# Kernel optimization log

Hardware: AMD Instinct MI355X
Metric: run time of the kernel (lower is better)

## Reference

```python
import jax, jax.numpy as jnp
import numpy as np

HIDDEN = 896
N_HEADS = 14
N_KV = 2
HEAD_DIM = HIDDEN // N_HEADS  # 64
N_REP = N_HEADS // N_KV       # 7
ROPE_THETA = 1000000.0


def setup_inputs() -> dict:
    key = jax.random.key(0)
    ks = jax.random.split(key, 8)
    B, S = 2, 2048
    s = 0.02
    return {
        "hidden_states": jax.random.normal(ks[0], (B, S, HIDDEN), dtype=jnp.float32),
        "position_ids": jnp.broadcast_to(jnp.arange(S, dtype=jnp.int64), (B, S)),
        "Wq": jax.random.normal(ks[1], (HIDDEN, HIDDEN), dtype=jnp.float32) * s,
        "bq": jnp.zeros((HIDDEN,), dtype=jnp.float32),
        "Wk": jax.random.normal(ks[2], (N_KV * HEAD_DIM, HIDDEN), dtype=jnp.float32) * s,
        "bk": jnp.zeros((N_KV * HEAD_DIM,), dtype=jnp.float32),
        "Wv": jax.random.normal(ks[3], (N_KV * HEAD_DIM, HIDDEN), dtype=jnp.float32) * s,
        "bv": jnp.zeros((N_KV * HEAD_DIM,), dtype=jnp.float32),
        "Wo": jax.random.normal(ks[4], (HIDDEN, HIDDEN), dtype=jnp.float32) * s,
    }


def _rotate_half(x):
    x1, x2 = x[..., : HEAD_DIM // 2], x[..., HEAD_DIM // 2 :]
    return jnp.concatenate((-x2, x1), axis=-1)


def reference(hidden_states, position_ids, Wq, bq, Wk, bk, Wv, bv, Wo):
    B, S, _ = hidden_states.shape
    q = (hidden_states @ Wq.T + bq).reshape(B, S, N_HEADS, HEAD_DIM)
    k = (hidden_states @ Wk.T + bk).reshape(B, S, N_KV, HEAD_DIM)
    v = (hidden_states @ Wv.T + bv).reshape(B, S, N_KV, HEAD_DIM)

    # RoPE: cos/sin [B, S, 1, HEAD_DIM]
    inv_freq = 1.0 / (ROPE_THETA ** (jnp.arange(0, HEAD_DIM, 2, dtype=jnp.float32) / HEAD_DIM))
    freqs = position_ids.astype(jnp.float32)[..., None] * inv_freq  # [B,S,D/2]
    emb = jnp.concatenate((freqs, freqs), axis=-1)
    cos = jnp.cos(emb)[:, :, None, :]
    sin = jnp.sin(emb)[:, :, None, :]
    q = q * cos + _rotate_half(q) * sin
    k = k * cos + _rotate_half(k) * sin

    # [B, H, S, D]; repeat KV heads (GQA)
    q = q.transpose(0, 2, 1, 3)
    k = jnp.repeat(k.transpose(0, 2, 1, 3), N_REP, axis=1)
    v = jnp.repeat(v.transpose(0, 2, 1, 3), N_REP, axis=1)

    scale = 1.0 / np.sqrt(HEAD_DIM)
    scores = jnp.einsum("bhqd,bhkd->bhqk", q, k) * scale
    causal = jnp.tril(jnp.ones((S, S), dtype=bool))
    scores = jnp.where(causal[None, None, :, :], scores, jnp.finfo(scores.dtype).min)
    probs = jax.nn.softmax(scores, axis=-1)
    attn = jnp.einsum("bhqk,bhkd->bhqd", probs, v)  # [B,H,S,D]
    attn = attn.transpose(0, 2, 1, 3).reshape(B, S, HIDDEN)
    return attn @ Wo.T
```

## Files before the change

kernel.cpp:

```cpp
#include <hip/hip_runtime.h>

#define HID 896
#define NH 14
#define NKV 2
#define NREP 7
#define SEQ 2048
#define BT 2
#define NTOK (BT*SEQ)
#define CSCALE 0.18033688011112042f

typedef __attribute__((ext_vector_type(8))) short bf16x8;
typedef __attribute__((ext_vector_type(8))) unsigned short u16x8;
typedef __attribute__((ext_vector_type(4))) float fx4;
typedef __attribute__((ext_vector_type(4))) short s16x4;
typedef _Float16 f16x4 __attribute__((ext_vector_type(4)));
typedef __fp16 fp16x2 __attribute__((ext_vector_type(2)));

__device__ __forceinline__ unsigned short f2b(float x){
  union { float f; unsigned u; } a; a.f = x;
  unsigned r = a.u + 0x7FFFu + ((a.u >> 16) & 1u);
  return (unsigned short)(r >> 16);
}
__device__ __forceinline__ unsigned short f2h(float x){
  union { _Float16 h; unsigned short u; } a; a.h = (_Float16)x; return a.u;
}
__device__ __forceinline__ u16x8 cvt8(float4 a, float4 b){
  u16x8 o;
  o[0]=f2b(a.x); o[1]=f2b(a.y); o[2]=f2b(a.z); o[3]=f2b(a.w);
  o[4]=f2b(b.x); o[5]=f2b(b.y); o[6]=f2b(b.z); o[7]=f2b(b.w);
  return o;
}

__global__ __launch_bounds__(256) void qkv_gemm_kernel(
    const float* __restrict__ hidden,
    const float* __restrict__ Wq, const float* __restrict__ Wk, const float* __restrict__ Wv,
    const float* __restrict__ bq, const float* __restrict__ bk, const float* __restrict__ bv,
    const int* __restrict__ pos,
    unsigned short* __restrict__ qo, unsigned short* __restrict__ ko,
    unsigned short* __restrict__ vt)
{
  __shared__ short As[64*72];
  __shared__ short Bs[128*72];
  const int tid = threadIdx.x;
  const int bm = blockIdx.x, bn = blockIdx.y;
  const int w = tid >> 6, l = tid & 63, l15 = l & 15, q4 = l >> 4;
  const int wm = w >> 1, wn = w & 1;

  fx4 acc[2][4] = {};

  const float* Wsrc = (bn < 7) ? Wq + (size_t)(bn*128)*HID : ((bn == 7) ? Wk : Wv);

  const int srow = tid >> 3, scol = (tid & 7)*8;
  const float* Agf = hidden + (size_t)(bm*64 + srow)*HID + scol;
  const float* Bgf = Wsrc + (size_t)srow*HID + scol;

  float4 a0[2], a1[2], b0[4], b1[4];
#pragma unroll
  for (int p = 0; p < 2; p++){
    a0[p] = *(const float4*)(Agf + (size_t)p*32*HID);
    a1[p] = *(const float4*)(Agf + (size_t)p*32*HID + 4);
  }
#pragma unroll
  for (int p = 0; p < 4; p++){
    b0[p] = *(const float4*)(Bgf + (size_t)p*32*HID);
    b1[p] = *(const float4*)(Bgf + (size_t)p*32*HID + 4);
  }

  for (int kt = 0; kt < 14; kt++){
#pragma unroll
    for (int p = 0; p < 2; p++)
      *(u16x8*)&As[(srow + p*32)*72 + scol] = cvt8(a0[p], a1[p]);
#pragma unroll
    for (int p = 0; p < 4; p++)
      *(u16x8*)&Bs[(srow + p*32)*72 + scol] = cvt8(b0[p], b1[p]);
    __syncthreads();
    if (kt < 13){
      const int ko_ = (kt+1)*64;
#pragma unroll
      for (int p = 0; p < 2; p++){
        a0[p] = *(const float4*)(Agf + (size_t)p*32*HID + ko_);
        a1[p] = *(const float4*)(Agf + (size_t)p*32*HID + ko_ + 4);
      }
#pragma unroll
      for (int p = 0; p < 4; p++){
        b0[p] = *(const float4*)(Bgf + (size_t)p*32*HID + ko_);
        b1[p] = *(const float4*)(Bgf + (size_t)p*32*HID + ko_ + 4);
      }
    }
#pragma unroll
    for (int ks = 0; ks < 2; ks++){
      bf16x8 af[2], bf[4];
#pragma unroll
      for (int mt = 0; mt < 2; mt++)
        af[mt] = *(bf16x8*)&As[(wm*32 + mt*16 + l15)*72 + ks*32 + q4*8];
#pragma unroll
      for (int nt = 0; nt < 4; nt++)
        bf[nt] = *(bf16x8*)&Bs[(wn*64 + nt*16 + l15)*72 + ks*32 + q4*8];
#pragma unroll
      for (int mt = 0; mt < 2; mt++)
#pragma unroll
        for (int nt = 0; nt < 4; nt++)
          acc[mt][nt] = __builtin_amdgcn_mfma_f32_16x16x32_bf16(af[mt], bf[nt], acc[mt][nt], 0,0,0);
    }
    __syncthreads();
  }

  const int hu = bn*2 + wn;
  const float* bias; int kind, hloc;
  if (hu < NH)      { bias = bq + hu*64;      kind = 0; hloc = hu; }
  else if (hu < 16) { bias = bk + (hu-NH)*64; kind = 1; hloc = hu-NH; }
  else              { bias = bv + (hu-16)*64; kind = 2; hloc = hu-16; }
  float bl[4];
#pragma unroll
  for (int nt = 0; nt < 4; nt++) bl[nt] = bias[nt*16 + l15];

  if (kind == 2){
#pragma unroll
    for (int mt = 0; mt < 2; mt++)
#pragma unroll
      for (int j = 0; j < 4; j++){
        int grow = bm*64 + wm*32 + mt*16 + q4*4 + j;
        int b = grow >> 11, s = grow & (SEQ-1);
        int tile = s >> 6, key = s & 63;
        unsigned short* dst = vt + (size_t)(((b*NKV + hloc)*(SEQ/64) + tile)*4096);
#pragma unroll
        for (int nt = 0; nt < 4; nt++)
          dst[(nt*16 + l15)*64 + key] = f2h(acc[mt][nt][j] + bl[nt]);
      }
  } else {
    const float qs = (kind == 0) ? CSCALE : 1.0f;
    float invf[2];
#pragma unroll
    for (int nt = 0; nt < 2; nt++)
      invf[nt] = exp2f(-(float)(nt*16 + l15) * 0.62286151779138041f);
#pragma unroll
    for (int mt = 0; mt < 2; mt++)
#pragma unroll
      for (int j = 0; j < 4; j++){
        int grow = bm*64 + wm*32 + mt*16 + q4*4 + j;
        int b = grow >> 11, s = grow & (SEQ-1);
        float p = (float)pos[grow];
        unsigned short* dst = (kind == 0)
            ? qo + ((size_t)(b*NH  + hloc)*SEQ + s)*64
            : ko + ((size_t)(b*NKV + hloc)*SEQ + s)*64;
        float x1 = acc[mt][0][j] + bl[0], x2 = acc[mt][2][j] + bl[2];
        float y1 = acc[mt][1][j] + bl[1], y2 = acc[mt][3][j] + bl[3];
        float s0v, c0v, s1v, c1v;
        sincosf(p*invf[0], &s0v, &c0v);
        sincosf(p*invf[1], &s1v, &c1v);
        dst[l15]      = f2b((x1*c0v - x2*s0v)*qs);
        dst[16 + l15] = f2b((y1*c1v - y2*s1v)*qs);
        dst[32 + l15] = f2b((x2*c0v + x1*s0v)*qs);
        dst[48 + l15] = f2b((y2*c1v + y1*s1v)*qs);
      }
  }
}

__device__ __forceinline__ void smax_pv(
    const fx4* s, bool diag, int wl, int q4,
    float& m_run, float& l_run, fx4* o, const f16x4 vf[4][4])
{
  float tv[16];
#pragma unroll
  for (int tl = 0; tl < 4; tl++)
#pragma unroll
    for (int j = 0; j < 4; j++){
      float x = s[tl][j];
      if (diag && (tl*16 + q4*4 + j > wl)) x = -1e30f;
      tv[tl*4+j] = x;
    }
  float mx = tv[0];
#pragma unroll
  for (int i = 1; i < 16; i++) mx = fmaxf(mx, tv[i]);
  mx = fmaxf(mx, __shfl_xor(mx, 16));
  mx = fmaxf(mx, __shfl_xor(mx, 32));
  float mn = fmaxf(m_run, mx);
  float al = exp2f(m_run - mn);
  m_run = mn;
  float p[16], rs = 0.f;
#pragma unroll
  for (int i = 0; i < 16; i++){ p[i] = exp2f(tv[i] - mn); rs += p[i]; }
  rs += __shfl_xor(rs, 16);
  rs += __shfl_xor(rs, 32);
  l_run = l_run*al + rs;
#pragma unroll
  for (int nt = 0; nt < 4; nt++)
#pragma unroll
    for (int j = 0; j < 4; j++) o[nt][j] *= al;
  f16x4 pf[4];
#pragma unroll
  for (int tl = 0; tl < 4; tl++){
    union { f16x4 v; fp16x2 h[2]; } u;
    u.h[0] = __builtin_amdgcn_cvt_pkrtz(p[tl*4+0], p[tl*4+1]);
    u.h[1] = __builtin_amdgcn_cvt_pkrtz(p[tl*4+2], p[tl*4+3]);
    pf[tl] = u.v;
  }
#pragma unroll
  for (int nt = 0; nt < 4; nt++)
#pragma unroll
    for (int tl = 0; tl < 4; tl++)
      o[nt] = __builtin_amdgcn_mfma_f32_16x16x16f16(vf[nt][tl], pf[tl], o[nt], 0,0,0);
}

__global__ __launch_bounds__(512) void attn_kernel(
    const unsigned short* __restrict__ q, const unsigned short* __restrict__ k,
    const unsigned short* __restrict__ vt, unsigned short* __restrict__ ao)
{
  __shared__ short SB[4*64*72];
  short* KsB = SB;
  short* VtB = SB + 2*64*72;

  const int tid = threadIdx.x;
  const int w = tid >> 6, l = tid & 63, l15 = l & 15, q4 = l >> 4;
  const int g = w >> 2, wi = w & 3;
  const int tlo = blockIdx.x, thi = 31 - tlo;
  const int h = blockIdx.y, b = blockIdx.z, kvh = h / NREP;
  const int wl = wi*16 + l15;

  const unsigned short* qbase = q + ((size_t)(b*NH + h)*SEQ)*64;
  const unsigned short* qpA = qbase + (size_t)(thi*64 + wl)*64;
  const unsigned short* qpB = qbase + (size_t)(tlo*64 + wl)*64;
  bf16x8 qA0 = *(const bf16x8*)(qpA + q4*8), qA1 = *(const bf16x8*)(qpA + 32 + q4*8);
  bf16x8 qB0 = *(const bf16x8*)(qpB + q4*8), qB1 = *(const bf16x8*)(qpB + 32 + q4*8);

  fx4 oA[4] = {}, oB[4] = {};
  float mA = -1e30f, lA = 0.f, mB = -1e30f, lB = 0.f;

  const unsigned short* kbase = k  + ((size_t)(b*NKV + kvh)*SEQ)*64;
  const unsigned short* vbase = vt + (size_t)((b*NKV + kvh)*(SEQ/64))*4096;

  const int P = (thi + 2) >> 1;

  u16x8 kreg[2], vreg[2];
#pragma unroll
  for (int p = 0; p < 2; p++){
    int idx = p*512 + tid, tile = idx >> 9, off = idx & 511;
    kreg[p] = *(const u16x8*)(kbase + (size_t)tile*4096 + off*8);
    vreg[p] = *(const u16x8*)(vbase + (size_t)tile*4096 + off*8);
  }

  for (int si = 0; si < P; si++){
#pragma unroll
    for (int p = 0; p < 2; p++){
      int idx = p*512 + tid, tile = idx >> 9, off = idx & 511;
      int rr = off >> 3, g8 = off & 7;
      *(u16x8*)&KsB[tile*4608 + rr*72 + g8*8] = kreg[p];
      *(u16x8*)&VtB[tile*4608 + rr*72 + g8*8] = vreg[p];
    }
    __syncthreads();

    if (si + 1 < P){
      const int k0n = 2*(si+1);
#pragma unroll
      for (int p = 0; p < 2; p++){
        int idx = p*512 + tid, tile = idx >> 9, off = idx & 511;
        int tk = k0n + tile; if (tk > thi) tk = thi;
        kreg[p] = *(const u16x8*)(kbase + (size_t)tk*4096 + off*8);
        vreg[p] = *(const u16x8*)(vbase + (size_t)tk*4096 + off*8);
      }
    }

    const int kt = 2*si + g;
    if (kt <= thi){
      const short* Kst = KsB + g*4608;
      const short* Vtt = VtB + g*4608;
      bf16x8 kf0[4], kf1[4];
#pragma unroll
      for (int tl = 0; tl < 4; tl++){
        kf0[tl] = *(const bf16x8*)&Kst[(tl*16 + l15)*72 + q4*8];
        kf1[tl] = *(const bf16x8*)&Kst[(tl*16 + l15)*72 + 32 + q4*8];
      }
      f16x4 vf[4][4];
#pragma unroll
      for (int nt = 0; nt < 4; nt++)
#pragma unroll
        for (int tl = 0; tl < 4; tl++)
          vf[nt][tl] = *(const f16x4*)&Vtt[(nt*16 + l15)*72 + tl*16 + q4*4];

      {
        fx4 s[4] = {};
#pragma unroll
        for (int tl = 0; tl < 4; tl++){
          s[tl] = __builtin_amdgcn_mfma_f32_16x16x32_bf16(kf0[tl], qA0, s[tl], 0,0,0);
          s[tl] = __builtin_amdgcn_mfma_f32_16x16x32_bf16(kf1[tl], qA1, s[tl], 0,0,0);
        }
        smax_pv(s, kt == thi, wl, q4, mA, lA, oA, vf);
      }
      if (kt <= tlo){
        fx4 s[4] = {};
#pragma unroll
        for (int tl = 0; tl < 4; tl++){
          s[tl] = __builtin_amdgcn_mfma_f32_16x16x32_bf16(kf0[tl], qB0, s[tl], 0,0,0);
          s[tl] = __builtin_amdgcn_mfma_f32_16x16x32_bf16(kf1[tl], qB1, s[tl], 0,0,0);
        }
        smax_pv(s, kt == tlo, wl, q4, mB, lB, oB, vf);
      }
    }
    __syncthreads();
  }

  float* F = (float*)SB;
  if (g == 1){
    float* fa = F + (((wi*2 + 0)*64 + l)*18);
#pragma unroll
    for (int nt = 0; nt < 4; nt++)
#pragma unroll
      for (int j = 0; j < 4; j++) fa[nt*4 + j] = oA[nt][j];
    fa[16] = mA; fa[17] = lA;
    float* fb = F + (((wi*2 + 1)*64 + l)*18);
#pragma unroll
    for (int nt = 0; nt < 4; nt++)
#pragma unroll
      for (int j = 0; j < 4; j++) fb[nt*4 + j] = oB[nt][j];
    fb[16] = mB; fb[17] = lB;
  }
  __syncthreads();
  if (g == 0){
    {
      const float* fa = F + (((wi*2 + 0)*64 + l)*18);
      float m1 = fa[16], l1 = fa[17];
      float mM = fmaxf(mA, m1);
      float a0 = exp2f(mA - mM), a1 = exp2f(m1 - mM);
      lA = lA*a0 + l1*a1;
#pragma unroll
      for (int nt = 0; nt < 4; nt++)
#pragma unroll
        for (int j = 0; j < 4; j++) oA[nt][j] = oA[nt][j]*a0 + fa[nt*4+j]*a1;
    }
    {
      const float* fb = F + (((wi*2 + 1)*64 + l)*18);
      float m1 = fb[16], l1 = fb[17];
      float mM = fmaxf(mB, m1);
      float a0 = exp2f(mB - mM), a1 = exp2f(m1 - mM);
      lB = lB*a0 + l1*a1;
#pragma unroll
      for (int nt = 0; nt < 4; nt++)
#pragma unroll
        for (int j = 0; j < 4; j++) oB[nt][j] = oB[nt][j]*a0 + fb[nt*4+j]*a1;
    }
    {
      float inv = 1.0f / lA;
      unsigned short* dst = ao + ((size_t)(b*SEQ + thi*64 + wl))*HID + h*64;
#pragma unroll
      for (int nt = 0; nt < 4; nt++){
        s16x4 ov;
        ov[0] = (short)f2b(oA[nt][0]*inv); ov[1] = (short)f2b(oA[nt][1]*inv);
        ov[2] = (short)f2b(oA[nt][2]*inv); ov[3] = (short)f2b(oA[nt][3]*inv);
        *(s16x4*)(dst + nt*16 + q4*4) = ov;
      }
    }
    {
      float inv = 1.0f / lB;
      unsigned short* dst = ao + ((size_t)(b*SEQ + tlo*64 + wl))*HID + h*64;
#pragma unroll
      for (int nt = 0; nt < 4; nt++){
        s16x4 ov;
        ov[0] = (short)f2b(oB[nt][0]*inv); ov[1] = (short)f2b(oB[nt][1]*inv);
        ov[2] = (short)f2b(oB[nt][2]*inv); ov[3] = (short)f2b(oB[nt][3]*inv);
        *(s16x4*)(dst + nt*16 + q4*4) = ov;
      }
    }
  }
}

__global__ __launch_bounds__(256) void out_gemm_kernel(
    const unsigned short* __restrict__ A, const float* __restrict__ Wo,
    float* __restrict__ out)
{
  __shared__ short As[64*72];
  __shared__ short Bs[128*72];
  const int tid = threadIdx.x;
  const int bm = blockIdx.x, bn = blockIdx.y;
  const int w = tid >> 6, l = tid & 63, l15 = l & 15, q4 = l >> 4;
  const int wm = w >> 1, wn = w & 1;

  fx4 acc[2][4] = {};

  const int srow = tid >> 3, scol = (tid & 7)*8;
  const unsigned short* Ag = A + (size_t)(bm*64 + srow)*HID + scol;
  const float* Bgf = Wo + (size_t)(bn*128 + srow)*HID + scol;

  u16x8 ar[2]; float4 b0[4], b1[4];
#pragma unroll
  for (int p = 0; p < 2; p++) ar[p] = *(const u16x8*)(Ag + (size_t)p*32*HID);
#pragma unroll
  for (int p = 0; p < 4; p++){
    b0[p] = *(const float4*)(Bgf + (size_t)p*32*HID);
    b1[p] = *(const float4*)(Bgf + (size_t)p*32*HID + 4);
  }

  for (int kt = 0; kt < 14; kt++){
#pragma unroll
    for (int p = 0; p < 2; p++) *(u16x8*)&As[(srow + p*32)*72 + scol] = ar[p];
#pragma unroll
    for (int p = 0; p < 4; p++) *(u16x8*)&Bs[(srow + p*32)*72 + scol] = cvt8(b0[p], b1[p]);
    __syncthreads();
    if (kt < 13){
      const int ko_ = (kt+1)*64;
#pragma unroll
      for (int p = 0; p < 2; p++) ar[p] = *(const u16x8*)(Ag + (size_t)p*32*HID + ko_);
#pragma unroll
      for (int p = 0; p < 4; p++){
        b0[p] = *(const float4*)(Bgf + (size_t)p*32*HID + ko_);
        b1[p] = *(const float4*)(Bgf + (size_t)p*32*HID + ko_ + 4);
      }
    }
#pragma unroll
    for (int ks = 0; ks < 2; ks++){
      bf16x8 af[2], bf[4];
#pragma unroll
      for (int mt = 0; mt < 2; mt++)
        af[mt] = *(bf16x8*)&As[(wm*32 + mt*16 + l15)*72 + ks*32 + q4*8];
#pragma unroll
      for (int nt = 0; nt < 4; nt++)
        bf[nt] = *(bf16x8*)&Bs[(wn*64 + nt*16 + l15)*72 + ks*32 + q4*8];
#pragma unroll
      for (int mt = 0; mt < 2; mt++)
#pragma unroll
        for (int nt = 0; nt < 4; nt++)
          acc[mt][nt] = __builtin_amdgcn_mfma_f32_16x16x32_bf16(af[mt], bf[nt], acc[mt][nt], 0,0,0);
    }
    __syncthreads();
  }

#pragma unroll
  for (int mt = 0; mt < 2; mt++)
#pragma unroll
    for (int j = 0; j < 4; j++){
      int grow = bm*64 + wm*32 + mt*16 + q4*4 + j;
      float* dst = out + (size_t)grow*HID + bn*128 + wn*64;
#pragma unroll
      for (int nt = 0; nt < 4; nt++)
        dst[nt*16 + l15] = acc[mt][nt][j];
    }
}

extern "C" void kernel_launch(void* const* d_in, const int* in_sizes, int n_in,
                              void* d_out, int out_size, void* d_ws, size_t ws_size,
                              hipStream_t stream)
{
  const float* hidden = (const float*)d_in[0];
  const int*   pos    = (const int*)d_in[1];
  const float* Wq = (const float*)d_in[2]; const float* bq = (const float*)d_in[3];
  const float* Wk = (const float*)d_in[4]; const float* bk = (const float*)d_in[5];
  const float* Wv = (const float*)d_in[6]; const float* bv = (const float*)d_in[7];
  const float* Wo = (const float*)d_in[8];

  unsigned short* qws  = (unsigned short*)d_ws;
  unsigned short* kws  = qws  + (size_t)BT*NH*SEQ*64;
  unsigned short* vtws = kws  + (size_t)BT*NKV*SEQ*64;
  unsigned short* aws  = vtws + (size_t)BT*NKV*SEQ*64;

  qkv_gemm_kernel<<<dim3(NTOK/64, 9), 256, 0, stream>>>(
      hidden, Wq, Wk, Wv, bq, bk, bv, pos, qws, kws, vtws);

  attn_kernel<<<dim3(16, NH, BT), 512, 0, stream>>>(qws, kws, vtws, aws);

  out_gemm_kernel<<<dim3(NTOK/64, 7), 256, 0, stream>>>(aws, Wo, (float*)d_out);
}
```

Before: 175.2 us.

## Prepack operands to bf16 MFMA fragment layout and drop LDS staging in GEMMs

Adds a pre-pass that converts hidden states and all weight matrices to bf16 stored in MFMA fragment order. The QKV and output GEMMs then load fragments straight from global memory with register double-buffering, with no shared memory or barriers. The attention kernel writes its output directly in the packed A layout for the output projection. This removes repeated fp32 loads and conversion inside the GEMM loops, but adds an extra kernel launch and pass over memory and loses intra-block data sharing through LDS.

```diff
diff --git a/kernel.cpp b/kernel.cpp
--- a/kernel.cpp
+++ b/kernel.cpp
@@ -7,6 +7,7 @@
 #define SEQ 2048
 #define BT 2
 #define NTOK (BT*SEQ)
+#define KT32 (HID/32)
 #define CSCALE 0.18033688011112042f
 
 typedef __attribute__((ext_vector_type(8))) short bf16x8;
@@ -31,78 +32,83 @@
   return o;
 }
 
-__global__ __launch_bounds__(256) void qkv_gemm_kernel(
+__global__ __launch_bounds__(256) void cvt_pack_kernel(
     const float* __restrict__ hidden,
     const float* __restrict__ Wq, const float* __restrict__ Wk, const float* __restrict__ Wv,
+    const float* __restrict__ Wo,
+    unsigned short* __restrict__ apk, unsigned short* __restrict__ bpkq,
+    unsigned short* __restrict__ bpko)
+{
+  const int job = blockIdx.y;
+  const int n = (job == 0) ? 256*KT32*64 : (job == 1 ? 72*KT32*64 : 56*KT32*64);
+  unsigned short* dst = (job == 0) ? apk : (job == 1 ? bpkq : bpko);
+
+  for (int i = blockIdx.x*256 + threadIdx.x; i < n; i += gridDim.x*256){
+    int l = i & 63, kt = (i >> 6) % KT32, blk = i / (KT32*64);
+    int col = kt*32 + (l >> 4)*8;
+    const float* src;
+    if (job == 0){
+      src = hidden + (size_t)(blk*16 + (l & 15))*HID + col;
+    } else if (job == 1){
+      const float* W; int r;
+      if (blk < 56)      { W = Wq; r = blk*16; }
+      else if (blk < 64) { W = Wk; r = (blk-56)*16; }
+      else               { W = Wv; r = (blk-64)*16; }
+      src = W + (size_t)(r + (l & 15))*HID + col;
+    } else {
+      src = Wo + (size_t)(blk*16 + (l & 15))*HID + col;
+    }
+    float4 a = *(const float4*)src;
+    float4 b = *(const float4*)(src + 4);
+    *(u16x8*)(dst + (size_t)i*8) = cvt8(a, b);
+  }
+}
+
+__global__ __launch_bounds__(256) void qkv_gemm_kernel(
+    const unsigned short* __restrict__ Apk, const unsigned short* __restrict__ Bpk,
     const float* __restrict__ bq, const float* __restrict__ bk, const float* __restrict__ bv,
     const int* __restrict__ pos,
     unsigned short* __restrict__ qo, unsigned short* __restrict__ ko,
     unsigned short* __restrict__ vt)
 {
-  __shared__ short As[64*72];
-  __shared__ short Bs[128*72];
   const int tid = threadIdx.x;
   const int bm = blockIdx.x, bn = blockIdx.y;
   const int w = tid >> 6, l = tid & 63, l15 = l & 15, q4 = l >> 4;
   const int wm = w >> 1, wn = w & 1;
+  const int mb0 = bm*4 + wm*2, nb0 = bn*8 + wn*4;
 
   fx4 acc[2][4] = {};
 
-  const float* Wsrc = (bn < 7) ? Wq + (size_t)(bn*128)*HID : ((bn == 7) ? Wk : Wv);
-
-  const int srow = tid >> 3, scol = (tid & 7)*8;
-  const float* Agf = hidden + (size_t)(bm*64 + srow)*HID + scol;
-  const float* Bgf = Wsrc + (size_t)srow*HID + scol;
-
-  float4 a0[2], a1[2], b0[4], b1[4];
-#pragma unroll
-  for (int p = 0; p < 2; p++){
-    a0[p] = *(const float4*)(Agf + (size_t)p*32*HID);
-    a1[p] = *(const float4*)(Agf + (size_t)p*32*HID + 4);
-  }
-#pragma unroll
-  for (int p = 0; p < 4; p++){
-    b0[p] = *(const float4*)(Bgf + (size_t)p*32*HID);
-    b1[p] = *(const float4*)(Bgf + (size_t)p*32*HID + 4);
-  }
-
-  for (int kt = 0; kt < 14; kt++){
-#pragma unroll
-    for (int p = 0; p < 2; p++)
-      *(u16x8*)&As[(srow + p*32)*72 + scol] = cvt8(a0[p], a1[p]);
-#pragma unroll
-    for (int p = 0; p < 4; p++)
-      *(u16x8*)&Bs[(srow + p*32)*72 + scol] = cvt8(b0[p], b1[p]);
-    __syncthreads();
-    if (kt < 13){
-      const int ko_ = (kt+1)*64;
-#pragma unroll
-      for (int p = 0; p < 2; p++){
-        a0[p] = *(const float4*)(Agf + (size_t)p*32*HID + ko_);
-        a1[p] = *(const float4*)(Agf + (size_t)p*32*HID + ko_ + 4);
-      }
-#pragma unroll
-      for (int p = 0; p < 4; p++){
-        b0[p] = *(const float4*)(Bgf + (size_t)p*32*HID + ko_);
-        b1[p] = *(const float4*)(Bgf + (size_t)p*32*HID + ko_ + 4);
-      }
-    }
-#pragma unroll
-    for (int ks = 0; ks < 2; ks++){
-      bf16x8 af[2], bf[4];
-#pragma unroll
-      for (int mt = 0; mt < 2; mt++)
-        af[mt] = *(bf16x8*)&As[(wm*32 + mt*16 + l15)*72 + ks*32 + q4*8];
-#pragma unroll
-      for (int nt = 0; nt < 4; nt++)
-        bf[nt] = *(bf16x8*)&Bs[(wn*64 + nt*16 + l15)*72 + ks*32 + q4*8];
-#pragma unroll
-      for (int mt = 0; mt < 2; mt++)
-#pragma unroll
-        for (int nt = 0; nt < 4; nt++)
-          acc[mt][nt] = __builtin_amdgcn_mfma_f32_16x16x32_bf16(af[mt], bf[nt], acc[mt][nt], 0,0,0);
-    }
-    __syncthreads();
+  const unsigned short* Ab[2];
+  const unsigned short* Bb[4];
+#pragma unroll
+  for (int mt = 0; mt < 2; mt++) Ab[mt] = Apk + ((size_t)(mb0+mt)*KT32)*512 + l*8;
+#pragma unroll
+  for (int nt = 0; nt < 4; nt++) Bb[nt] = Bpk + ((size_t)(nb0+nt)*KT32)*512 + l*8;
+
+  bf16x8 ac[2], bc[4], an[2], bnx[4];
+#pragma unroll
+  for (int mt = 0; mt < 2; mt++) ac[mt] = *(const bf16x8*)(Ab[mt]);
+#pragma unroll
+  for (int nt = 0; nt < 4; nt++) bc[nt] = *(const bf16x8*)(Bb[nt]);
+
+  for (int kt = 0; kt < KT32; kt++){
+    if (kt < KT32-1){
+      const int off = (kt+1)*512;
+#pragma unroll
+      for (int mt = 0; mt < 2; mt++) an[mt]  = *(const bf16x8*)(Ab[mt] + off);
+#pragma unroll
+      for (int nt = 0; nt < 4; nt++) bnx[nt] = *(const bf16x8*)(Bb[nt] + off);
+    }
+#pragma unroll
+    for (int mt = 0; mt < 2; mt++)
+#pragma unroll
+      for (int nt = 0; nt < 4; nt++)
+        acc[mt][nt] = __builtin_amdgcn_mfma_f32_16x16x32_bf16(ac[mt], bc[nt], acc[mt][nt], 0,0,0);
+#pragma unroll
+    for (int mt = 0; mt < 2; mt++) ac[mt] = an[mt];
+#pragma unroll
+    for (int nt = 0; nt < 4; nt++) bc[nt] = bnx[nt];
   }
 
   const int hu = bn*2 + wn;
@@ -202,9 +208,24 @@
       o[nt] = __builtin_amdgcn_mfma_f32_16x16x16f16(vf[nt][tl], pf[tl], o[nt], 0,0,0);
 }
 
+__device__ __forceinline__ void store_packedA(
+    unsigned short* apk, int mb, int h, int q4, int l15, const fx4* o, float inv)
+{
+#pragma unroll
+  for (int nt = 0; nt < 4; nt++){
+    s16x4 ov;
+    ov[0] = (short)f2b(o[nt][0]*inv); ov[1] = (short)f2b(o[nt][1]*inv);
+    ov[2] = (short)f2b(o[nt][2]*inv); ov[3] = (short)f2b(o[nt][3]*inv);
+    int ktile = h*2 + (nt >> 1);
+    int flane = 16*((nt & 1)*2 + (q4 >> 1)) + l15;
+    size_t addr = ((size_t)(mb*KT32 + ktile)*64 + flane)*8 + (q4 & 1)*4;
+    *(s16x4*)(apk + addr) = ov;
+  }
+}
+
 __global__ __launch_bounds__(512) void attn_kernel(
     const unsigned short* __restrict__ q, const unsigned short* __restrict__ k,
-    const unsigned short* __restrict__ vt, unsigned short* __restrict__ ao)
+    const unsigned short* __restrict__ vt, unsigned short* __restrict__ apk)
 {
   __shared__ short SB[4*64*72];
   short* KsB = SB;
@@ -338,89 +359,53 @@
 #pragma unroll
         for (int j = 0; j < 4; j++) oB[nt][j] = oB[nt][j]*a0 + fb[nt*4+j]*a1;
     }
-    {
-      float inv = 1.0f / lA;
-      unsigned short* dst = ao + ((size_t)(b*SEQ + thi*64 + wl))*HID + h*64;
-#pragma unroll
-      for (int nt = 0; nt < 4; nt++){
-        s16x4 ov;
-        ov[0] = (short)f2b(oA[nt][0]*inv); ov[1] = (short)f2b(oA[nt][1]*inv);
-        ov[2] = (short)f2b(oA[nt][2]*inv); ov[3] = (short)f2b(oA[nt][3]*inv);
-        *(s16x4*)(dst + nt*16 + q4*4) = ov;
-      }
-    }
-    {
-      float inv = 1.0f / lB;
-      unsigned short* dst = ao + ((size_t)(b*SEQ + tlo*64 + wl))*HID + h*64;
-#pragma unroll
-      for (int nt = 0; nt < 4; nt++){
-        s16x4 ov;
-        ov[0] = (short)f2b(oB[nt][0]*inv); ov[1] = (short)f2b(oB[nt][1]*inv);
-        ov[2] = (short)f2b(oB[nt][2]*inv); ov[3] = (short)f2b(oB[nt][3]*inv);
-        *(s16x4*)(dst + nt*16 + q4*4) = ov;
-      }
-    }
+    store_packedA(apk, b*128 + thi*4 + wi, h, q4, l15, oA, 1.0f/lA);
+    store_packedA(apk, b*128 + tlo*4 + wi, h, q4, l15, oB, 1.0f/lB);
   }
 }
 
 __global__ __launch_bounds__(256) void out_gemm_kernel(
-    const unsigned short* __restrict__ A, const float* __restrict__ Wo,
+    const unsigned short* __restrict__ Apk, const unsigned short* __restrict__ Bpk,
     float* __restrict__ out)
 {
-  __shared__ short As[64*72];
-  __shared__ short Bs[128*72];
   const int tid = threadIdx.x;
   const int bm = blockIdx.x, bn = blockIdx.y;
   const int w = tid >> 6, l = tid & 63, l15 = l & 15, q4 = l >> 4;
   const int wm = w >> 1, wn = w & 1;
+  const int mb0 = bm*4 + wm*2, nb0 = bn*8 + wn*4;
 
   fx4 acc[2][4] = {};
 
-  const int srow = tid >> 3, scol = (tid & 7)*8;
-  const unsigned short* Ag = A + (size_t)(bm*64 + srow)*HID + scol;
-  const float* Bgf = Wo + (size_t)(bn*128 + srow)*HID + scol;
-
-  u16x8 ar[2]; float4 b0[4], b1[4];
-#pragma unroll
-  for (int p = 0; p < 2; p++) ar[p] = *(const u16x8*)(Ag + (size_t)p*32*HID);
-#pragma unroll
-  for (int p = 0; p < 4; p++){
-    b0[p] = *(const float4*)(Bgf + (size_t)p*32*HID);
-    b1[p] = *(const float4*)(Bgf + (size_t)p*32*HID + 4);
-  }
-
-  for (int kt = 0; kt < 14; kt++){
-#pragma unroll
-    for (int p = 0; p < 2; p++) *(u16x8*)&As[(srow + p*32)*72 + scol] = ar[p];
-#pragma unroll
-    for (int p = 0; p < 4; p++) *(u16x8*)&Bs[(srow + p*32)*72 + scol] = cvt8(b0[p], b1[p]);
-    __syncthreads();
-    if (kt < 13){
-      const int ko_ = (kt+1)*64;
-#pragma unroll
-      for (int p = 0; p < 2; p++) ar[p] = *(const u16x8*)(Ag + (size_t)p*32*HID + ko_);
-#pragma unroll
-      for (int p = 0; p < 4; p++){
-        b0[p] = *(const float4*)(Bgf + (size_t)p*32*HID + ko_);
-        b1[p] = *(const float4*)(Bgf + (size_t)p*32*HID + ko_ + 4);
-      }
-    }
-#pragma unroll
-    for (int ks = 0; ks < 2; ks++){
-      bf16x8 af[2], bf[4];
-#pragma unroll
-      for (int mt = 0; mt < 2; mt++)
-        af[mt] = *(bf16x8*)&As[(wm*32 + mt*16 + l15)*72 + ks*32 + q4*8];
-#pragma unroll
-      for (int nt = 0; nt < 4; nt++)
-        bf[nt] = *(bf16x8*)&Bs[(wn*64 + nt*16 + l15)*72 + ks*32 + q4*8];
-#pragma unroll
-      for (int mt = 0; mt < 2; mt++)
-#pragma unroll
-        for (int nt = 0; nt < 4; nt++)
-          acc[mt][nt] = __builtin_amdgcn_mfma_f32_16x16x32_bf16(af[mt], bf[nt], acc[mt][nt], 0,0,0);
-    }
-    __syncthreads();
+  const unsigned short* Ab[2];
+  const unsigned short* Bb[4];
+#pragma unroll
+  for (int mt = 0; mt < 2; mt++) Ab[mt] = Apk + ((size_t)(mb0+mt)*KT32)*512 + l*8;
+#pragma unroll
+  for (int nt = 0; nt < 4; nt++) Bb[nt] = Bpk + ((size_t)(nb0+nt)*KT32)*512 + l*8;
+
+  bf16x8 ac[2], bc[4], an[2], bnx[4];
+#pragma unroll
+  for (int mt = 0; mt < 2; mt++) ac[mt] = *(const bf16x8*)(Ab[mt]);
+#pragma unroll
+  for (int nt = 0; nt < 4; nt++) bc[nt] = *(const bf16x8*)(Bb[nt]);
+
+  for (int kt = 0; kt < KT32; kt++){
+    if (kt < KT32-1){
+      const int off = (kt+1)*512;
+#pragma unroll
+      for (int mt = 0; mt < 2; mt++) an[mt]  = *(const bf16x8*)(Ab[mt] + off);
+#pragma unroll
+      for (int nt = 0; nt < 4; nt++) bnx[nt] = *(const bf16x8*)(Bb[nt] + off);
+    }
+#pragma unroll
+    for (int mt = 0; mt < 2; mt++)
+#pragma unroll
+      for (int nt = 0; nt < 4; nt++)
+        acc[mt][nt] = __builtin_amdgcn_mfma_f32_16x16x32_bf16(ac[mt], bc[nt], acc[mt][nt], 0,0,0);
+#pragma unroll
+    for (int mt = 0; mt < 2; mt++) ac[mt] = an[mt];
+#pragma unroll
+    for (int nt = 0; nt < 4; nt++) bc[nt] = bnx[nt];
   }
 
 #pragma unroll
@@ -449,12 +434,17 @@
   unsigned short* qws  = (unsigned short*)d_ws;
   unsigned short* kws  = qws  + (size_t)BT*NH*SEQ*64;
   unsigned short* vtws = kws  + (size_t)BT*NKV*SEQ*64;
-  unsigned short* aws  = vtws + (size_t)BT*NKV*SEQ*64;
+  unsigned short* apk  = vtws + (size_t)BT*NKV*SEQ*64;
+  unsigned short* bpkq = apk  + (size_t)NTOK*HID;
+  unsigned short* bpko = bpkq + (size_t)1152*HID;
+
+  cvt_pack_kernel<<<dim3(224, 3), 256, 0, stream>>>(
+      hidden, Wq, Wk, Wv, Wo, apk, bpkq, bpko);
 
   qkv_gemm_kernel<<<dim3(NTOK/64, 9), 256, 0, stream>>>(
-      hidden, Wq, Wk, Wv, bq, bk, bv, pos, qws, kws, vtws);
-
-  attn_kernel<<<dim3(16, NH, BT), 512, 0, stream>>>(qws, kws, vtws, aws);
-
-  out_gemm_kernel<<<dim3(NTOK/64, 7), 256, 0, stream>>>(aws, Wo, (float*)d_out);
-}
+      apk, bpkq, bq, bk, bv, pos, qws, kws, vtws);
+
+  attn_kernel<<<dim3(16, NH, BT), 512, 0, stream>>>(qws, kws, vtws, apk);
+
+  out_gemm_kernel<<<dim3(NTOK/64, 7), 256, 0, stream>>>(apk, bpko, (float*)d_out);
+}
```

After: 173.5 us. About the same (-0.9%).
